# Performance work log

Hardware: AMD Instinct MI355X
Metric: run time of the kernel (lower is better)

The kernel has to match this reference:

```python
import jax, jax.numpy as jnp
import numpy as np
import math

WIN = (2, 7, 7)      # (wd, wh, ww) 3D window
SHIFT = (1, 3, 3)    # cyclic shift per dim
HEADS = 4
DIM = 128
MLP_HIDDEN = 4 * DIM


def _layernorm(x, w, b, eps=1e-5):
    m = x.mean(-1, keepdims=True)
    v = jnp.var(x, axis=-1, keepdims=True)
    return (x - m) * jax.lax.rsqrt(v + eps) * w + b


def setup_inputs() -> dict:
    key = jax.random.key(0)
    ks = jax.random.split(key, 6)
    C, H = DIM, MLP_HIDDEN
    p = lambda k, shape: jax.random.normal(k, shape, jnp.float32) * 0.02
    return {
        "x": jax.random.normal(ks[0], (4, 8, 56, 56, C), jnp.float32),
        "norm1_w": jnp.ones((C,), jnp.float32),
        "norm1_b": jnp.zeros((C,), jnp.float32),
        "qkv_w": p(ks[1], (C, 3 * C)),
        "qkv_b": jnp.zeros((3 * C,), jnp.float32),
        "proj_w": p(ks[2], (C, C)),
        "proj_b": jnp.zeros((C,), jnp.float32),
        "norm2_w": jnp.ones((C,), jnp.float32),
        "norm2_b": jnp.zeros((C,), jnp.float32),
        "fc1_w": p(ks[3], (C, H)),
        "fc1_b": jnp.zeros((H,), jnp.float32),
        "fc2_w": p(ks[4], (H, C)),
        "fc2_b": jnp.zeros((C,), jnp.float32),
    }


def reference(x, norm1_w, norm1_b, qkv_w, qkv_b, proj_w, proj_b,
              norm2_w, norm2_b, fc1_w, fc1_b, fc2_w, fc2_b):
    B, D, H, W, C = x.shape
    wd, wh, ww = WIN
    sd, sh, sw = SHIFT
    nd, nh, nw = D // wd, H // wh, W // ww
    N = wd * wh * ww          # tokens per window (98)
    hd = C // HEADS
    scale = 1.0 / math.sqrt(hd)

    # ---- part1: norm1 -> cyclic shift -> window partition -> MHA -> reverse ----
    h = _layernorm(x, norm1_w, norm1_b)
    h = jnp.roll(h, (-sd, -sh, -sw), axis=(1, 2, 3))
    # window partition: (B,D,H,W,C) -> (B*nWindows, N, C)
    xw = h.reshape(B, nd, wd, nh, wh, nw, ww, C)
    xw = xw.transpose(0, 1, 3, 5, 2, 4, 6, 7).reshape(-1, N, C)

    qkv = (xw @ qkv_w + qkv_b).reshape(-1, N, 3, HEADS, hd).transpose(2, 0, 3, 1, 4)
    q, k, v = qkv[0], qkv[1], qkv[2]      # each (Bw, heads, N, hd)
    scores = jnp.einsum('bhnc,bhmc->bhnm', q, k) * scale
    attn = jax.nn.softmax(scores, axis=-1)
    out = jnp.einsum('bhnm,bhmc->bhnc', attn, v)
    out = out.transpose(0, 2, 1, 3).reshape(-1, N, C)
    out = out @ proj_w + proj_b

    # window reverse: (B*nWindows, N, C) -> (B,D,H,W,C)
    out = out.reshape(B, nd, nh, nw, wd, wh, ww, C)
    out = out.transpose(0, 1, 4, 2, 5, 3, 6, 7).reshape(B, D, H, W, C)
    out = jnp.roll(out, (sd, sh, sw), axis=(1, 2, 3))

    x = x + out  # residual (drop_path = identity)

    # ---- part2: norm2 -> MLP (Linear -> SiLU -> Linear) -> residual ----
    h2 = _layernorm(x, norm2_w, norm2_b)
    h2 = jax.nn.silu(h2 @ fc1_w + fc1_b) @ fc2_w + fc2_b
    return x + h2
```

## Files before the change

### kernel.cpp

```cpp
#include <hip/hip_runtime.h>

typedef unsigned short u16;
typedef unsigned int u32;
typedef __bf16 bf16x8 __attribute__((ext_vector_type(8)));
typedef float f32x4 __attribute__((ext_vector_type(4)));
typedef u16 u16x8 __attribute__((ext_vector_type(8)));
typedef u16 u16x2 __attribute__((ext_vector_type(2)));

__device__ __forceinline__ float bf2f(u16 u) {
    union { u32 u; float f; } c; c.u = ((u32)u) << 16; return c.f;
}
__device__ __forceinline__ u16 f2bf(float f) {
    union { float f; u32 u; } c; c.f = f;
    u32 r = c.u + 0x7fffu + ((c.u >> 16) & 1u);
    return (u16)(r >> 16);
}
__device__ __forceinline__ bf16x8 ld_frag(const u16* p) {
    return *reinterpret_cast<const bf16x8*>(p);
}

__global__ __launch_bounds__(256) void k_wT(
    const float* __restrict__ qkv_w, const float* __restrict__ proj_w,
    const float* __restrict__ fc1_w, const float* __restrict__ fc2_w,
    u16* __restrict__ qkvT, u16* __restrict__ projT,
    u16* __restrict__ fc1T, u16* __restrict__ fc2T)
{
    int t = blockIdx.x * 256 + threadIdx.x;
    if (t < 49152) { int k = t / 384, n = t % 384; qkvT[n*128 + k] = f2bf(qkv_w[t]); }
    if (t < 16384) { int k = t / 128, n = t % 128; projT[n*128 + k] = f2bf(proj_w[t]); }
    if (t < 65536) { int k = t / 512, n = t % 512; fc1T[n*128 + k] = f2bf(fc1_w[t]); }
    if (t < 65536) { int k = t / 128, n = t % 128; fc2T[n*512 + k] = f2bf(fc2_w[t]); }
}

__global__ __launch_bounds__(256) void k_ln1_part(
    const float* __restrict__ x, const float* __restrict__ w, const float* __restrict__ b,
    u16* __restrict__ xw)
{
    int wv = threadIdx.x >> 6, l = threadIdx.x & 63;
    int g = blockIdx.x * 4 + wv;
    int wi = g / 98, n = g % 98;
    int iw = wi & 7, ih = (wi >> 3) & 7, id = (wi >> 6) & 3, bb = wi >> 8;
    int tw = n % 7, tt = n / 7, th = tt % 7, td = tt / 7;
    int d  = (id * 2 + td + 1) & 7;
    int hh = ih * 7 + th + 3; if (hh >= 56) hh -= 56;
    int ww = iw * 7 + tw + 3; if (ww >= 56) ww -= 56;
    long src = ((((long)bb * 8 + d) * 56 + hh) * 56 + ww) * 128;
    float2 v = *(const float2*)(x + src + l * 2);
    float f0 = v.x, f1 = v.y;
    float s = f0 + f1, s2 = f0*f0 + f1*f1;
    #pragma unroll
    for (int o = 32; o; o >>= 1) { s += __shfl_xor(s, o); s2 += __shfl_xor(s2, o); }
    float mean = s * (1.f/128.f);
    float var  = s2 * (1.f/128.f) - mean*mean;
    float rstd = rsqrtf(var + 1e-5f);
    float y0 = (f0 - mean) * rstd * w[l*2]   + b[l*2];
    float y1 = (f1 - mean) * rstd * w[l*2+1] + b[l*2+1];
    u16x2 o2; o2[0] = f2bf(y0); o2[1] = f2bf(y1);
    *(u16x2*)(xw + (long)g * 128 + l * 2) = o2;
}

__global__ __launch_bounds__(256) void k_gemm128(
    const u16* __restrict__ A, const u16* __restrict__ BT,
    const float* __restrict__ bias, u16* __restrict__ out, int ldo)
{
    __shared__ __align__(16) u16 la[128*136];
    __shared__ __align__(16) u16 lb[128*136];
    int m0 = blockIdx.x * 128, n0 = blockIdx.y * 128;
    int t = threadIdx.x;
    #pragma unroll
    for (int i = 0; i < 8; i++) {
        int u = t + i * 256;
        int r = u >> 4, c = u & 15;
        *(u16x8*)&la[r*136 + c*8] = *(const u16x8*)&A [(long)(m0 + r)*128 + c*8];
        *(u16x8*)&lb[r*136 + c*8] = *(const u16x8*)&BT[(long)(n0 + r)*128 + c*8];
    }
    __syncthreads();
    int wv = t >> 6, l = t & 63;
    int wm = (wv & 1) * 64, wn = (wv >> 1) * 64;
    int lr = l & 15, lk = (l >> 4) * 8;
    f32x4 acc[4][4] = {};
    #pragma unroll
    for (int kk = 0; kk < 4; kk++) {
        bf16x8 af[4], bfr[4];
        #pragma unroll
        for (int mi = 0; mi < 4; mi++) af[mi]  = ld_frag(&la[(wm + mi*16 + lr)*136 + kk*32 + lk]);
        #pragma unroll
        for (int ni = 0; ni < 4; ni++) bfr[ni] = ld_frag(&lb[(wn + ni*16 + lr)*136 + kk*32 + lk]);
        #pragma unroll
        for (int mi = 0; mi < 4; mi++)
            #pragma unroll
            for (int ni = 0; ni < 4; ni++)
                acc[mi][ni] = __builtin_amdgcn_mfma_f32_16x16x32_bf16(af[mi], bfr[ni], acc[mi][ni], 0, 0, 0);
    }
    int rb = (l >> 4) * 4;
    #pragma unroll
    for (int mi = 0; mi < 4; mi++)
        #pragma unroll
        for (int ni = 0; ni < 4; ni++) {
            int col = n0 + wn + ni*16 + lr;
            float bv = bias[col];
            #pragma unroll
            for (int r = 0; r < 4; r++) {
                int row = m0 + wm + mi*16 + rb + r;
                out[(long)row*ldo + col] = f2bf(acc[mi][ni][r] + bv);
            }
        }
}

__global__ __launch_bounds__(256) void k_attn(
    const u16* __restrict__ qkv, u16* __restrict__ attn_out)
{
    __shared__ __align__(16) u16 lq[128*40];
    __shared__ __align__(16) u16 lk[128*40];
    __shared__ __align__(16) u16 lvt[32*136];
    __shared__ __align__(16) u16 lp[4][16*136];
    int wi = blockIdx.x, h = blockIdx.y;
    int t = threadIdx.x;
    int wv = t >> 6, l = t & 63;
    const long base = (long)wi * 98 * 384 + h * 32;
    u16* lpw = lp[wv];
    {
        u16x8 z8 = {};
        for (int i = l; i < 272; i += 64) *(u16x8*)&lpw[i*8] = z8;
    }
    #pragma unroll
    for (int i = 0; i < 4; i++) {
        int u = t + i * 256;
        int mat = u >> 9, row = (u >> 2) & 127, ch = u & 3;
        u16x8 v = {};
        if (row < 98) v = *(const u16x8*)&qkv[base + (long)row*384 + mat*128 + ch*8];
        u16* dst = mat ? lk : lq;
        *(u16x8*)&dst[row*40 + ch*8] = v;
    }
    #pragma unroll
    for (int i = 0; i < 2; i++) {
        int u = t + i * 256;
        int row = u >> 2, ch = u & 3;
        u16x8 v = {};
        if (row < 98) v = *(const u16x8*)&qkv[base + (long)row*384 + 256 + ch*8];
        #pragma unroll
        for (int j = 0; j < 8; j++) lvt[(ch*8 + j)*136 + row] = v[j];
    }
    __syncthreads();
    int lr = l & 15, lg = l >> 4, lkk = lg * 8;
    const float scale = 0.17677669529663687f;
    for (int rt = wv; rt < 7; rt += 4) {
        bf16x8 qa = ld_frag(&lq[(rt*16 + lr)*40 + lkk]);
        f32x4 s[7];
        #pragma unroll
        for (int ct = 0; ct < 7; ct++) {
            bf16x8 kb = ld_frag(&lk[(ct*16 + lr)*40 + lkk]);
            f32x4 zz = {0.f, 0.f, 0.f, 0.f};
            s[ct] = __builtin_amdgcn_mfma_f32_16x16x32_bf16(qa, kb, zz, 0, 0, 0);
        }
        #pragma unroll
        for (int ct = 0; ct < 7; ct++) {
            bool valid = (ct < 6) || (lr < 2);
            #pragma unroll
            for (int r = 0; r < 4; r++)
                s[ct][r] = valid ? s[ct][r] * scale : -1e30f;
        }
        f32x4 mx;
        #pragma unroll
        for (int r = 0; r < 4; r++) {
            float m = s[0][r];
            #pragma unroll
            for (int ct = 1; ct < 7; ct++) m = fmaxf(m, s[ct][r]);
            #pragma unroll
            for (int o = 1; o < 16; o <<= 1) m = fmaxf(m, __shfl_xor(m, o));
            mx[r] = m;
        }
        f32x4 sum = {0.f, 0.f, 0.f, 0.f};
        #pragma unroll
        for (int ct = 0; ct < 7; ct++)
            #pragma unroll
            for (int r = 0; r < 4; r++) {
                s[ct][r] = __expf(s[ct][r] - mx[r]);
                sum[r] += s[ct][r];
            }
        #pragma unroll
        for (int r = 0; r < 4; r++) {
            float ss = sum[r];
            #pragma unroll
            for (int o = 1; o < 16; o <<= 1) ss += __shfl_xor(ss, o);
            sum[r] = 1.f / ss;
        }
        #pragma unroll
        for (int ct = 0; ct < 7; ct++)
            #pragma unroll
            for (int r = 0; r < 4; r++)
                lpw[(lg*4 + r)*136 + ct*16 + lr] = f2bf(s[ct][r] * sum[r]);
        #pragma unroll
        for (int ni = 0; ni < 2; ni++) {
            f32x4 acc = {0.f, 0.f, 0.f, 0.f};
            #pragma unroll
            for (int kk = 0; kk < 4; kk++) {
                bf16x8 pa = ld_frag(&lpw[lr*136 + kk*32 + lkk]);
                bf16x8 vb = ld_frag(&lvt[(ni*16 + lr)*136 + kk*32 + lkk]);
                acc = __builtin_amdgcn_mfma_f32_16x16x32_bf16(pa, vb, acc, 0, 0, 0);
            }
            #pragma unroll
            for (int r = 0; r < 4; r++) {
                int row = rt*16 + lg*4 + r;
                if (row < 98)
                    attn_out[((long)wi*98 + row)*128 + h*32 + ni*16 + lr] = f2bf(acc[r]);
            }
        }
    }
}

__global__ __launch_bounds__(256) void k_res_ln2(
    const u16* __restrict__ proj_out, const float* __restrict__ x,
    const float* __restrict__ w2, const float* __restrict__ b2,
    float* __restrict__ x1, u16* __restrict__ h2out)
{
    int wv = threadIdx.x >> 6, l = threadIdx.x & 63;
    int g = blockIdx.x * 4 + wv;
    int ww = g % 56; int t1 = g / 56;
    int hh = t1 % 56; int t2 = t1 / 56;
    int d = t2 & 7, bb = t2 >> 3;
    int d2 = (d + 7) & 7;
    int hs = hh - 3; if (hs < 0) hs += 56;
    int ws_ = ww - 3; if (ws_ < 0) ws_ += 56;
    int id = d2 >> 1, td = d2 & 1;
    int ih = hs / 7, th = hs % 7;
    int iw = ws_ / 7, tw = ws_ % 7;
    int wi = ((bb*4 + id)*8 + ih)*8 + iw;
    int n  = (td*7 + th)*7 + tw;
    long prow = ((long)wi*98 + n) * 128;
    long nrow = (long)g * 128;
    u16x2 pv = *(const u16x2*)&proj_out[prow + l*2];
    float2 xv = *(const float2*)&x[nrow + l*2];
    float v0 = bf2f(pv[0]) + xv.x;
    float v1 = bf2f(pv[1]) + xv.y;
    float2 o; o.x = v0; o.y = v1;
    *(float2*)&x1[nrow + l*2] = o;
    float s = v0 + v1, s2 = v0*v0 + v1*v1;
    #pragma unroll
    for (int o2 = 32; o2; o2 >>= 1) { s += __shfl_xor(s, o2); s2 += __shfl_xor(s2, o2); }
    float mean = s * (1.f/128.f), var = s2 * (1.f/128.f) - mean*mean;
    float rstd = rsqrtf(var + 1e-5f);
    float y0 = (v0 - mean)*rstd*w2[l*2]   + b2[l*2];
    float y1 = (v1 - mean)*rstd*w2[l*2+1] + b2[l*2+1];
    u16x2 oh; oh[0] = f2bf(y0); oh[1] = f2bf(y1);
    *(u16x2*)&h2out[nrow + l*2] = oh;
}

__global__ __launch_bounds__(256, 4) void k_mlp(
    const u16* __restrict__ h2, const u16* __restrict__ fc1T, const float* __restrict__ b1,
    const u16* __restrict__ fc2T, const float* __restrict__ b2,
    const float* __restrict__ x1, float* __restrict__ out)
{
    __shared__ __align__(16) u16 lh[64*136];
    __shared__ __align__(16) u16 lhc[2][64*72];
    int m0 = blockIdx.x * 64;
    int t = threadIdx.x;
    int wv = t >> 6, l = t & 63;
    int lr = l & 15, lg = l >> 4, lk = lg * 8;
    #pragma unroll
    for (int i = 0; i < 4; i++) {
        int u = t + i * 256;
        int r = u >> 4, c = u & 15;
        *(u16x8*)&lh[r*136 + c*8] = *(const u16x8*)&h2[(long)(m0 + r)*128 + c*8];
    }
    __syncthreads();
    f32x4 oacc[4][2] = {};
    for (int ch = 0; ch < 8; ch++) {
        u16* lc = lhc[ch & 1];
        int un0 = ch*64 + wv*16;
        bf16x8 bfr[4];
        #pragma unroll
        for (int kk = 0; kk < 4; kk++)
            bfr[kk] = ld_frag(&fc1T[(un0 + lr)*128 + kk*32 + lk]);
        float bv = b1[un0 + lr];
        #pragma unroll
        for (int mt = 0; mt < 4; mt++) {
            f32x4 acc = {0.f, 0.f, 0.f, 0.f};
            #pragma unroll
            for (int kk = 0; kk < 4; kk++) {
                bf16x8 a = ld_frag(&lh[(mt*16 + lr)*136 + kk*32 + lk]);
                acc = __builtin_amdgcn_mfma_f32_16x16x32_bf16(a, bfr[kk], acc, 0, 0, 0);
            }
            #pragma unroll
            for (int r = 0; r < 4; r++) {
                float v = acc[r] + bv;
                v = v / (1.f + __expf(-v));
                lc[(mt*16 + lg*4 + r)*72 + wv*16 + lr] = f2bf(v);
            }
        }
        __syncthreads();
        #pragma unroll
        for (int nt = 0; nt < 2; nt++) {
            int col = wv*32 + nt*16 + lr;
            bf16x8 b0 = ld_frag(&fc2T[(long)col*512 + ch*64 + lk]);
            bf16x8 b1f = ld_frag(&fc2T[(long)col*512 + ch*64 + 32 + lk]);
            #pragma unroll
            for (int mt = 0; mt < 4; mt++) {
                bf16x8 a0 = ld_frag(&lc[(mt*16 + lr)*72 + lk]);
                bf16x8 a1 = ld_frag(&lc[(mt*16 + lr)*72 + 32 + lk]);
                oacc[mt][nt] = __builtin_amdgcn_mfma_f32_16x16x32_bf16(a0, b0, oacc[mt][nt], 0, 0, 0);
                oacc[mt][nt] = __builtin_amdgcn_mfma_f32_16x16x32_bf16(a1, b1f, oacc[mt][nt], 0, 0, 0);
            }
        }
    }
    #pragma unroll
    for (int nt = 0; nt < 2; nt++) {
        int col = wv*32 + nt*16 + lr;
        float bv = b2[col];
        #pragma unroll
        for (int mt = 0; mt < 4; mt++) {
            #pragma unroll
            for (int r = 0; r < 4; r++) {
                int row = m0 + mt*16 + lg*4 + r;
                out[(long)row*128 + col] = oacc[mt][nt][r] + bv + x1[(long)row*128 + col];
            }
        }
    }
}

extern "C" void kernel_launch(void* const* d_in, const int* in_sizes, int n_in,
                              void* d_out, int out_size, void* d_ws, size_t ws_size,
                              hipStream_t stream)
{
    const float* x      = (const float*)d_in[0];
    const float* n1w    = (const float*)d_in[1];
    const float* n1b    = (const float*)d_in[2];
    const float* qkv_w  = (const float*)d_in[3];
    const float* qkv_b  = (const float*)d_in[4];
    const float* proj_w = (const float*)d_in[5];
    const float* proj_b = (const float*)d_in[6];
    const float* n2w    = (const float*)d_in[7];
    const float* n2b    = (const float*)d_in[8];
    const float* fc1_w  = (const float*)d_in[9];
    const float* fc1_b  = (const float*)d_in[10];
    const float* fc2_w  = (const float*)d_in[11];
    const float* fc2_b  = (const float*)d_in[12];
    float* out = (float*)d_out;

    u16* ws16  = (u16*)d_ws;
    u16* xw    = ws16;
    u16* qkv   = xw + 12845056;
    u16* qkvT  = qkv + 38535168;
    u16* projT = qkvT + 49152;
    u16* fc1T  = projT + 16384;
    u16* fc2T  = fc1T + 65536;

    k_wT<<<256, 256, 0, stream>>>(qkv_w, proj_w, fc1_w, fc2_w, qkvT, projT, fc1T, fc2T);
    k_ln1_part<<<25088, 256, 0, stream>>>(x, n1w, n1b, xw);
    dim3 gq(784, 3);
    k_gemm128<<<gq, 256, 0, stream>>>(xw, qkvT, qkv_b, qkv, 384);
    dim3 ga(1024, 4);
    k_attn<<<ga, 256, 0, stream>>>(qkv, xw);
    dim3 gp(784, 1);
    k_gemm128<<<gp, 256, 0, stream>>>(xw, projT, proj_b, qkv, 128);
    k_res_ln2<<<25088, 256, 0, stream>>>(qkv, x, n2w, n2b, out , xw );
    k_mlp<<<1568, 256, 0, stream>>>(xw , fc1T, fc1_b, fc2T, fc2_b, out , out);
}
```

Measured before the change: 212.7 us.

## Restructure MLP kernel so each wave owns 32 rows, removing block syncs

The fused MLP kernel now gives each wave its own 32-row slice. The wave keeps its h2 A-fragments in registers and computes all 512 hidden units and all 128 output columns itself, staging the SiLU activations in a private XOR-swizzled LDS buffer. This removes the block-wide __syncthreads between fc1 and fc2 and the shared h2 tile load, and halves the grid to 128 rows per block. In exchange each wave reloads the full fc1/fc2 weights from global memory or cache, and the larger accumulators raise register pressure (launch bounds lowered to 3).

```diff
diff --git a/kernel.cpp b/kernel.cpp
--- a/kernel.cpp
+++ b/kernel.cpp
@@ -246,75 +246,77 @@
     *(u16x2*)&h2out[nrow + l*2] = oh;
 }
 
-__global__ __launch_bounds__(256, 4) void k_mlp(
+__global__ __launch_bounds__(256, 3) void k_mlp(
     const u16* __restrict__ h2, const u16* __restrict__ fc1T, const float* __restrict__ b1,
     const u16* __restrict__ fc2T, const float* __restrict__ b2,
     const float* __restrict__ x1, float* __restrict__ out)
 {
-    __shared__ __align__(16) u16 lh[64*136];
-    __shared__ __align__(16) u16 lhc[2][64*72];
-    int m0 = blockIdx.x * 64;
+    __shared__ __align__(16) u16 lph[4][32*64];
     int t = threadIdx.x;
     int wv = t >> 6, l = t & 63;
     int lr = l & 15, lg = l >> 4, lk = lg * 8;
-    #pragma unroll
-    for (int i = 0; i < 4; i++) {
-        int u = t + i * 256;
-        int r = u >> 4, c = u & 15;
-        *(u16x8*)&lh[r*136 + c*8] = *(const u16x8*)&h2[(long)(m0 + r)*128 + c*8];
-    }
-    __syncthreads();
-    f32x4 oacc[4][2] = {};
+    u16* lp = lph[wv];
+    long rb = (long)blockIdx.x * 128 + wv * 32;
+    bf16x8 a[2][4];
+    #pragma unroll
+    for (int mt = 0; mt < 2; mt++)
+        #pragma unroll
+        for (int kk = 0; kk < 4; kk++)
+            a[mt][kk] = ld_frag(&h2[(rb + mt*16 + lr)*128 + kk*32 + lk]);
+    f32x4 oacc[2][8] = {};
     for (int ch = 0; ch < 8; ch++) {
-        u16* lc = lhc[ch & 1];
-        int un0 = ch*64 + wv*16;
-        bf16x8 bfr[4];
-        #pragma unroll
-        for (int kk = 0; kk < 4; kk++)
-            bfr[kk] = ld_frag(&fc1T[(un0 + lr)*128 + kk*32 + lk]);
-        float bv = b1[un0 + lr];
-        #pragma unroll
-        for (int mt = 0; mt < 4; mt++) {
-            f32x4 acc = {0.f, 0.f, 0.f, 0.f};
-            #pragma unroll
-            for (int kk = 0; kk < 4; kk++) {
-                bf16x8 a = ld_frag(&lh[(mt*16 + lr)*136 + kk*32 + lk]);
-                acc = __builtin_amdgcn_mfma_f32_16x16x32_bf16(a, bfr[kk], acc, 0, 0, 0);
-            }
+        #pragma unroll
+        for (int nt = 0; nt < 4; nt++) {
+            int u = ch*64 + nt*16;
+            bf16x8 bfr[4];
+            #pragma unroll
+            for (int kk = 0; kk < 4; kk++)
+                bfr[kk] = ld_frag(&fc1T[(u + lr)*128 + kk*32 + lk]);
+            float bv = b1[u + lr];
+            #pragma unroll
+            for (int mt = 0; mt < 2; mt++) {
+                f32x4 acc = {0.f, 0.f, 0.f, 0.f};
+                #pragma unroll
+                for (int kk = 0; kk < 4; kk++)
+                    acc = __builtin_amdgcn_mfma_f32_16x16x32_bf16(a[mt][kk], bfr[kk], acc, 0, 0, 0);
+                #pragma unroll
+                for (int r = 0; r < 4; r++) {
+                    float v = acc[r] + bv;
+                    v = v / (1.f + __expf(-v));
+                    int row = mt*16 + lg*4 + r;
+                    int byo = row*128 + (((nt*16 + lr)*2) ^ ((row & 7) << 4));
+                    *(u16*)((char*)lp + byo) = f2bf(v);
+                }
+            }
+        }
+        #pragma unroll
+        for (int kk2 = 0; kk2 < 2; kk2++) {
+            bf16x8 pa[2];
+            #pragma unroll
+            for (int mt = 0; mt < 2; mt++) {
+                int row = mt*16 + lr;
+                int byo = row*128 + ((kk2*64 + lg*16) ^ ((row & 7) << 4));
+                pa[mt] = *(const bf16x8*)((const char*)lp + byo);
+            }
+            #pragma unroll
+            for (int nt2 = 0; nt2 < 8; nt2++) {
+                bf16x8 vb = ld_frag(&fc2T[(long)(nt2*16 + lr)*512 + ch*64 + kk2*32 + lk]);
+                oacc[0][nt2] = __builtin_amdgcn_mfma_f32_16x16x32_bf16(pa[0], vb, oacc[0][nt2], 0, 0, 0);
+                oacc[1][nt2] = __builtin_amdgcn_mfma_f32_16x16x32_bf16(pa[1], vb, oacc[1][nt2], 0, 0, 0);
+            }
+        }
+    }
+    #pragma unroll
+    for (int nt2 = 0; nt2 < 8; nt2++) {
+        int col = nt2*16 + lr;
+        float bv = b2[col];
+        #pragma unroll
+        for (int mt = 0; mt < 2; mt++)
             #pragma unroll
             for (int r = 0; r < 4; r++) {
-                float v = acc[r] + bv;
-                v = v / (1.f + __expf(-v));
-                lc[(mt*16 + lg*4 + r)*72 + wv*16 + lr] = f2bf(v);
-            }
-        }
-        __syncthreads();
-        #pragma unroll
-        for (int nt = 0; nt < 2; nt++) {
-            int col = wv*32 + nt*16 + lr;
-            bf16x8 b0 = ld_frag(&fc2T[(long)col*512 + ch*64 + lk]);
-            bf16x8 b1f = ld_frag(&fc2T[(long)col*512 + ch*64 + 32 + lk]);
-            #pragma unroll
-            for (int mt = 0; mt < 4; mt++) {
-                bf16x8 a0 = ld_frag(&lc[(mt*16 + lr)*72 + lk]);
-                bf16x8 a1 = ld_frag(&lc[(mt*16 + lr)*72 + 32 + lk]);
-                oacc[mt][nt] = __builtin_amdgcn_mfma_f32_16x16x32_bf16(a0, b0, oacc[mt][nt], 0, 0, 0);
-                oacc[mt][nt] = __builtin_amdgcn_mfma_f32_16x16x32_bf16(a1, b1f, oacc[mt][nt], 0, 0, 0);
-            }
-        }
-    }
-    #pragma unroll
-    for (int nt = 0; nt < 2; nt++) {
-        int col = wv*32 + nt*16 + lr;
-        float bv = b2[col];
-        #pragma unroll
-        for (int mt = 0; mt < 4; mt++) {
-            #pragma unroll
-            for (int r = 0; r < 4; r++) {
-                int row = m0 + mt*16 + lg*4 + r;
-                out[(long)row*128 + col] = oacc[mt][nt][r] + bv + x1[(long)row*128 + col];
-            }
-        }
+                long row = rb + mt*16 + lg*4 + r;
+                out[row*128 + col] = oacc[mt][nt2][r] + bv + x1[row*128 + col];
+            }
     }
 }
 
@@ -354,5 +356,5 @@
     dim3 gp(784, 1);
     k_gemm128<<<gp, 256, 0, stream>>>(xw, projT, proj_b, qkv, 128);
     k_res_ln2<<<25088, 256, 0, stream>>>(qkv, x, n2w, n2b, out , xw );
-    k_mlp<<<1568, 256, 0, stream>>>(xw , fc1T, fc1_b, fc2T, fc2_b, out , out);
-}
+    k_mlp<<<784, 256, 0, stream>>>(xw , fc1T, fc1_b, fc2T, fc2_b, out , out);
+}
```

Result: slower. 301.4 us (+41.7%).

## Fuse QKV projection into windowed attention kernel, one block per window

Applied to the files above, without the earlier changes.

The separate QKV GEMM launch is removed. Each attention block now loads its window's normalized tokens into LDS once, then for each head computes that head's Q, K and V with MFMA using weights read from global memory, and runs attention on them. This avoids writing and re-reading the 3x-wide qkv intermediate in HBM and drops one kernel launch. In exchange the grid shrinks from 4096 to 1024 blocks, the heads are processed serially with extra barriers, LDS use grows, and the attention output is written in place over xw, which other blocks do not read.

```diff
diff --git a/kernel.cpp b/kernel.cpp
--- a/kernel.cpp
+++ b/kernel.cpp
@@ -108,104 +108,119 @@
 }
 
 __global__ __launch_bounds__(256) void k_attn(
-    const u16* __restrict__ qkv, u16* __restrict__ attn_out)
-{
-    __shared__ __align__(16) u16 lq[128*40];
-    __shared__ __align__(16) u16 lk[128*40];
+    const u16* xw, const u16* __restrict__ qkvT,
+    const float* __restrict__ qkv_b, u16* attn_out)
+{
+    __shared__ __align__(16) u16 lxw[112*136];
+    __shared__ __align__(16) u16 lq[112*40];
+    __shared__ __align__(16) u16 lk[112*40];
     __shared__ __align__(16) u16 lvt[32*136];
     __shared__ __align__(16) u16 lp[4][16*136];
-    int wi = blockIdx.x, h = blockIdx.y;
+    int wi = blockIdx.x;
     int t = threadIdx.x;
     int wv = t >> 6, l = t & 63;
-    const long base = (long)wi * 98 * 384 + h * 32;
+    int lr = l & 15, lg = l >> 4, lkk = lg * 8;
     u16* lpw = lp[wv];
-    {
-        u16x8 z8 = {};
-        for (int i = l; i < 272; i += 64) *(u16x8*)&lpw[i*8] = z8;
-    }
-    #pragma unroll
-    for (int i = 0; i < 4; i++) {
-        int u = t + i * 256;
-        int mat = u >> 9, row = (u >> 2) & 127, ch = u & 3;
-        u16x8 v = {};
-        if (row < 98) v = *(const u16x8*)&qkv[base + (long)row*384 + mat*128 + ch*8];
-        u16* dst = mat ? lk : lq;
-        *(u16x8*)&dst[row*40 + ch*8] = v;
-    }
-    #pragma unroll
-    for (int i = 0; i < 2; i++) {
-        int u = t + i * 256;
-        int row = u >> 2, ch = u & 3;
-        u16x8 v = {};
-        if (row < 98) v = *(const u16x8*)&qkv[base + (long)row*384 + 256 + ch*8];
-        #pragma unroll
-        for (int j = 0; j < 8; j++) lvt[(ch*8 + j)*136 + row] = v[j];
+    u16x8 z8 = {};
+    for (int i = l; i < 272; i += 64) *(u16x8*)&lpw[i*8] = z8;
+    for (int i = t; i < 544; i += 256) *(u16x8*)&lvt[i*8] = z8;
+    for (int u = t; u < 112*16; u += 256) {
+        int row = u >> 4, c = u & 15;
+        u16x8 v = z8;
+        if (row < 98) v = *(const u16x8*)&xw[((long)wi*98 + row)*128 + c*8];
+        *(u16x8*)&lxw[row*136 + c*8] = v;
     }
     __syncthreads();
-    int lr = l & 15, lg = l >> 4, lkk = lg * 8;
     const float scale = 0.17677669529663687f;
-    for (int rt = wv; rt < 7; rt += 4) {
-        bf16x8 qa = ld_frag(&lq[(rt*16 + lr)*40 + lkk]);
-        f32x4 s[7];
-        #pragma unroll
-        for (int ct = 0; ct < 7; ct++) {
-            bf16x8 kb = ld_frag(&lk[(ct*16 + lr)*40 + lkk]);
-            f32x4 zz = {0.f, 0.f, 0.f, 0.f};
-            s[ct] = __builtin_amdgcn_mfma_f32_16x16x32_bf16(qa, kb, zz, 0, 0, 0);
-        }
-        #pragma unroll
-        for (int ct = 0; ct < 7; ct++) {
-            bool valid = (ct < 6) || (lr < 2);
-            #pragma unroll
-            for (int r = 0; r < 4; r++)
-                s[ct][r] = valid ? s[ct][r] * scale : -1e30f;
-        }
-        f32x4 mx;
-        #pragma unroll
-        for (int r = 0; r < 4; r++) {
-            float m = s[0][r];
-            #pragma unroll
-            for (int ct = 1; ct < 7; ct++) m = fmaxf(m, s[ct][r]);
-            #pragma unroll
-            for (int o = 1; o < 16; o <<= 1) m = fmaxf(m, __shfl_xor(m, o));
-            mx[r] = m;
-        }
-        f32x4 sum = {0.f, 0.f, 0.f, 0.f};
-        #pragma unroll
-        for (int ct = 0; ct < 7; ct++)
-            #pragma unroll
-            for (int r = 0; r < 4; r++) {
-                s[ct][r] = __expf(s[ct][r] - mx[r]);
-                sum[r] += s[ct][r];
-            }
-        #pragma unroll
-        for (int r = 0; r < 4; r++) {
-            float ss = sum[r];
-            #pragma unroll
-            for (int o = 1; o < 16; o <<= 1) ss += __shfl_xor(ss, o);
-            sum[r] = 1.f / ss;
-        }
-        #pragma unroll
-        for (int ct = 0; ct < 7; ct++)
-            #pragma unroll
-            for (int r = 0; r < 4; r++)
-                lpw[(lg*4 + r)*136 + ct*16 + lr] = f2bf(s[ct][r] * sum[r]);
-        #pragma unroll
-        for (int ni = 0; ni < 2; ni++) {
+    for (int h = 0; h < 4; h++) {
+        for (int job = wv; job < 42; job += 4) {
+            int mat = job / 14, rem = job % 14, mt = rem >> 1, nt = rem & 1;
+            int ch = mat*128 + h*32 + nt*16 + lr;
+            bf16x8 bfr[4];
+            #pragma unroll
+            for (int kk = 0; kk < 4; kk++)
+                bfr[kk] = ld_frag(&qkvT[(long)ch*128 + kk*32 + lkk]);
             f32x4 acc = {0.f, 0.f, 0.f, 0.f};
             #pragma unroll
             for (int kk = 0; kk < 4; kk++) {
-                bf16x8 pa = ld_frag(&lpw[lr*136 + kk*32 + lkk]);
-                bf16x8 vb = ld_frag(&lvt[(ni*16 + lr)*136 + kk*32 + lkk]);
-                acc = __builtin_amdgcn_mfma_f32_16x16x32_bf16(pa, vb, acc, 0, 0, 0);
-            }
-            #pragma unroll
-            for (int r = 0; r < 4; r++) {
-                int row = rt*16 + lg*4 + r;
-                if (row < 98)
-                    attn_out[((long)wi*98 + row)*128 + h*32 + ni*16 + lr] = f2bf(acc[r]);
-            }
-        }
+                bf16x8 a = ld_frag(&lxw[(mt*16 + lr)*136 + kk*32 + lkk]);
+                acc = __builtin_amdgcn_mfma_f32_16x16x32_bf16(a, bfr[kk], acc, 0, 0, 0);
+            }
+            float bv = qkv_b[ch];
+            #pragma unroll
+            for (int r = 0; r < 4; r++) {
+                int row = mt*16 + lg*4 + r;
+                u16 val = f2bf(acc[r] + bv);
+                if (mat == 0)      lq[row*40 + nt*16 + lr] = val;
+                else if (mat == 1) lk[row*40 + nt*16 + lr] = val;
+                else               lvt[(nt*16 + lr)*136 + row] = val;
+            }
+        }
+        __syncthreads();
+        for (int rt = wv; rt < 7; rt += 4) {
+            bf16x8 qa = ld_frag(&lq[(rt*16 + lr)*40 + lkk]);
+            f32x4 s[7];
+            #pragma unroll
+            for (int ct = 0; ct < 7; ct++) {
+                bf16x8 kb = ld_frag(&lk[(ct*16 + lr)*40 + lkk]);
+                f32x4 zz = {0.f, 0.f, 0.f, 0.f};
+                s[ct] = __builtin_amdgcn_mfma_f32_16x16x32_bf16(qa, kb, zz, 0, 0, 0);
+            }
+            #pragma unroll
+            for (int ct = 0; ct < 7; ct++) {
+                bool valid = (ct < 6) || (lr < 2);
+                #pragma unroll
+                for (int r = 0; r < 4; r++)
+                    s[ct][r] = valid ? s[ct][r] * scale : -1e30f;
+            }
+            f32x4 mx;
+            #pragma unroll
+            for (int r = 0; r < 4; r++) {
+                float m = s[0][r];
+                #pragma unroll
+                for (int ct = 1; ct < 7; ct++) m = fmaxf(m, s[ct][r]);
+                #pragma unroll
+                for (int o = 1; o < 16; o <<= 1) m = fmaxf(m, __shfl_xor(m, o));
+                mx[r] = m;
+            }
+            f32x4 sum = {0.f, 0.f, 0.f, 0.f};
+            #pragma unroll
+            for (int ct = 0; ct < 7; ct++)
+                #pragma unroll
+                for (int r = 0; r < 4; r++) {
+                    s[ct][r] = __expf(s[ct][r] - mx[r]);
+                    sum[r] += s[ct][r];
+                }
+            #pragma unroll
+            for (int r = 0; r < 4; r++) {
+                float ss = sum[r];
+                #pragma unroll
+                for (int o = 1; o < 16; o <<= 1) ss += __shfl_xor(ss, o);
+                sum[r] = 1.f / ss;
+            }
+            #pragma unroll
+            for (int ct = 0; ct < 7; ct++)
+                #pragma unroll
+                for (int r = 0; r < 4; r++)
+                    lpw[(lg*4 + r)*136 + ct*16 + lr] = f2bf(s[ct][r] * sum[r]);
+            #pragma unroll
+            for (int ni = 0; ni < 2; ni++) {
+                f32x4 acc = {0.f, 0.f, 0.f, 0.f};
+                #pragma unroll
+                for (int kk = 0; kk < 4; kk++) {
+                    bf16x8 pa = ld_frag(&lpw[lr*136 + kk*32 + lkk]);
+                    bf16x8 vb = ld_frag(&lvt[(ni*16 + lr)*136 + kk*32 + lkk]);
+                    acc = __builtin_amdgcn_mfma_f32_16x16x32_bf16(pa, vb, acc, 0, 0, 0);
+                }
+                #pragma unroll
+                for (int r = 0; r < 4; r++) {
+                    int row = rt*16 + lg*4 + r;
+                    if (row < 98)
+                        attn_out[((long)wi*98 + row)*128 + h*32 + ni*16 + lr] = f2bf(acc[r]);
+                }
+            }
+        }
+        __syncthreads();
     }
 }
 
@@ -339,20 +354,17 @@
 
     u16* ws16  = (u16*)d_ws;
     u16* xw    = ws16;
-    u16* qkv   = xw + 12845056;
-    u16* qkvT  = qkv + 38535168;
+    u16* pout  = xw + 12845056;
+    u16* qkvT  = pout + 38535168;
     u16* projT = qkvT + 49152;
     u16* fc1T  = projT + 16384;
     u16* fc2T  = fc1T + 65536;
 
     k_wT<<<256, 256, 0, stream>>>(qkv_w, proj_w, fc1_w, fc2_w, qkvT, projT, fc1T, fc2T);
     k_ln1_part<<<25088, 256, 0, stream>>>(x, n1w, n1b, xw);
-    dim3 gq(784, 3);
-    k_gemm128<<<gq, 256, 0, stream>>>(xw, qkvT, qkv_b, qkv, 384);
-    dim3 ga(1024, 4);
-    k_attn<<<ga, 256, 0, stream>>>(qkv, xw);
+    k_attn<<<1024, 256, 0, stream>>>(xw, qkvT, qkv_b, xw);
     dim3 gp(784, 1);
-    k_gemm128<<<gp, 256, 0, stream>>>(xw, projT, proj_b, qkv, 128);
-    k_res_ln2<<<25088, 256, 0, stream>>>(qkv, x, n2w, n2b, out , xw );
+    k_gemm128<<<gp, 256, 0, stream>>>(xw, projT, proj_b, pout, 128);
+    k_res_ln2<<<25088, 256, 0, stream>>>(pout, x, n2w, n2b, out , xw );
     k_mlp<<<1568, 256, 0, stream>>>(xw , fc1T, fc1_b, fc2T, fc2_b, out , out);
 }
```

Measured after the change: 253.3 us. 1.19x slower.
